# Kernel optimization log

Measured on AMD Instinct MI355X. Metric: run time of the kernel, lower is better.

The kernel has to match this reference:

```python
import jax, jax.numpy as jnp
import numpy as np

B, S, D = 2, 2048, 1024
H, HD = 16, 64


def setup_inputs() -> dict:
    key = jax.random.key(0)
    ks = jax.random.split(key, 10)
    scale = 1.0 / np.sqrt(D)
    inputs_q = jax.random.normal(ks[0], (B, S, D), dtype=jnp.float32)
    inputs_kv = jax.random.normal(ks[1], (B, S, D), dtype=jnp.float32)
    # causal mask, broadcast over batch: True = attend
    mask = jnp.broadcast_to(jnp.tril(jnp.ones((S, S), dtype=bool)), (B, S, S))
    Wq = jax.random.normal(ks[2], (D, H * HD), dtype=jnp.float32) * scale
    bq = jnp.zeros((H * HD,), dtype=jnp.float32)
    Wk = jax.random.normal(ks[3], (D, H * HD), dtype=jnp.float32) * scale
    bk = jnp.zeros((H * HD,), dtype=jnp.float32)
    Wv = jax.random.normal(ks[4], (D, H * HD), dtype=jnp.float32) * scale
    bv = jnp.zeros((H * HD,), dtype=jnp.float32)
    Wo = jax.random.normal(ks[5], (H * HD, D), dtype=jnp.float32) * scale
    bo = jnp.zeros((D,), dtype=jnp.float32)
    return {"inputs_q": inputs_q, "inputs_kv": inputs_kv, "mask": mask,
            "Wq": Wq, "bq": bq, "Wk": Wk, "bk": bk, "Wv": Wv, "bv": bv,
            "Wo": Wo, "bo": bo}


def reference(inputs_q, inputs_kv, mask, Wq, bq, Wk, bk, Wv, bv, Wo, bo):
    b, s_q, _ = inputs_q.shape
    s_k = inputs_kv.shape[1]
    # projections -> [B, S, H, HD]
    q = (inputs_q @ Wq + bq).reshape(b, s_q, H, HD)
    k = (inputs_kv @ Wk + bk).reshape(b, s_k, H, HD)
    v = (inputs_kv @ Wv + bv).reshape(b, s_k, H, HD)
    q = q / jnp.sqrt(jnp.asarray(HD, dtype=q.dtype))
    # scores: [B, H, Sq, Sk]
    attn = jnp.einsum('bqhd,bkhd->bhqk', q, k)
    m = mask[:, None, :, :]  # [B,1,Sq,Sk] broadcast over heads
    attn = jnp.where(m, attn, jnp.asarray(-1e30, dtype=attn.dtype))
    attn = jax.nn.softmax(attn, axis=-1)
    # dropout_rate = 0.0, deterministic -> identity
    out = jnp.einsum('bhqk,bkhd->bqhd', attn, v).reshape(b, s_q, H * HD)
    return out @ Wo + bo
```

## Files before the change

kernel.cpp:

```cpp
#include <hip/hip_runtime.h>

typedef __attribute__((ext_vector_type(4))) float f32x4;
typedef __attribute__((ext_vector_type(8))) short bf16x8;
typedef unsigned short u16;
typedef unsigned int u32;

#define AS1 __attribute__((address_space(1)))
#define AS3 __attribute__((address_space(3)))

#define WAITVM(N) do{ asm volatile("s_waitcnt vmcnt(" #N ")" ::: "memory"); \
                      __builtin_amdgcn_sched_barrier(0); }while(0)
#define RAWBAR    do{ __builtin_amdgcn_s_barrier();                          \
                      __builtin_amdgcn_sched_barrier(0); }while(0)

__device__ __forceinline__ float fast_exp2(float x){
  return __builtin_amdgcn_exp2f(x);
}

__device__ __forceinline__ u16 f2bf(float x){
  u32 u = __float_as_uint(x);
  u += 0x7fffu + ((u >> 16) & 1u);
  return (u16)(u >> 16);
}
__device__ __forceinline__ u16 f2bf_fast(float x){
  return (u16)((__float_as_uint(x) + 0x8000u) >> 16);
}

__global__ __launch_bounds__(256) void cvt_qkv(const float* __restrict__ s0,
                                               const float* __restrict__ s1,
                                               u16* __restrict__ d0,
                                               u16* __restrict__ d1, int n4)
{
  int i = blockIdx.x * 256 + threadIdx.x;
  if (i >= n4) return;
  const float* src = blockIdx.y ? s1 : s0;
  u16* dst = blockIdx.y ? d1 : d0;
  float4 v = reinterpret_cast<const float4*>(src)[i];
  ushort4 o;
  o.x = f2bf(v.x); o.y = f2bf(v.y); o.z = f2bf(v.z); o.w = f2bf(v.w);
  reinterpret_cast<ushort4*>(dst)[i] = o;
}

__global__ __launch_bounds__(256) void transpose_cvt4(const float* __restrict__ W0,
                                                      const float* __restrict__ W1,
                                                      const float* __restrict__ W2,
                                                      const float* __restrict__ W3,
                                                      u16* __restrict__ dst)
{
  __shared__ float tile[32][33];
  const int z = blockIdx.z;
  const float* src = z == 0 ? W0 : z == 1 ? W1 : z == 2 ? W2 : W3;
  u16* d = dst + (size_t)z * 1024 * 1024;
  int tx = threadIdx.x & 31, ty = threadIdx.x >> 5;
  int k0 = blockIdx.x * 32, n0 = blockIdx.y * 32;
  for (int r = 0; r < 4; ++r)
    tile[ty + r * 8][tx] = src[(size_t)(k0 + ty + r * 8) * 1024 + n0 + tx];
  __syncthreads();
  for (int r = 0; r < 4; ++r)
    d[(size_t)(n0 + ty + r * 8) * 1024 + k0 + tx] = f2bf(tile[tx][ty + r * 8]);
}

__global__ __launch_bounds__(256) void gemm_qkv(const u16* __restrict__ Xq,
                                                const u16* __restrict__ Xkv,
                                                const u16* __restrict__ Wt,
                                                const float* __restrict__ bq,
                                                const float* __restrict__ bk,
                                                const float* __restrict__ bv,
                                                u16* __restrict__ Qb,
                                                u16* __restrict__ Kb,
                                                u16* __restrict__ Vt,
                                                int M, int K)
{
  __shared__ u16 lA[3][128 * 32];
  __shared__ u16 lB[3][128 * 32];
  const int tid = threadIdx.x;
  const int l = tid & 63, w = tid >> 6;
  const int wr = w >> 1, wc = w & 1;
  const int bm0 = blockIdx.x * 128, bn0 = blockIdx.y * 128;
  const int seg = bn0 >> 10;
  const int nloc0 = bn0 & 1023;
  const u16* A = seg ? Xkv : Xq;
  const float* bias = seg == 0 ? bq : seg == 1 ? bk : bv;
  const float scale = seg == 0 ? 0.125f * 1.44269504089f : 1.0f;
  const int lr = l & 15, lg = (l >> 4) * 8;

#define STAGE_G(BI, KK) do{                                                   \
  _Pragma("unroll") for (int c_ = 0; c_ < 2; ++c_){                           \
    int e_ = (c_ * 256 + tid) * 8;                                            \
    int row_ = e_ >> 5, col_ = e_ & 31;                                       \
    __builtin_amdgcn_global_load_lds(                                         \
        (const AS1 u32*)(A + (size_t)(bm0 + row_) * K + (KK) * 32 + col_),    \
        (AS3 u32*)(&lA[BI][e_]), 16, 0, 0);                                   \
    __builtin_amdgcn_global_load_lds(                                         \
        (const AS1 u32*)(Wt + (size_t)(bn0 + row_) * K + (KK) * 32 + col_),   \
        (AS3 u32*)(&lB[BI][e_]), 16, 0, 0);                                   \
  }                                                                           \
}while(0)

  f32x4 acc[4][4];
#pragma unroll
  for (int m = 0; m < 4; ++m)
#pragma unroll
    for (int n = 0; n < 4; ++n) acc[m][n] = (f32x4){0.f, 0.f, 0.f, 0.f};

  STAGE_G(0, 0);
  STAGE_G(1, 1);

#pragma unroll
  for (int k = 0; k < 32; ++k){
    const int cur = k % 3;
    if (k < 30){ STAGE_G((k + 2) % 3, k + 2); WAITVM(8); }
    else if (k == 30){ WAITVM(4); }
    else { WAITVM(0); }
    RAWBAR;

    bf16x8 aF[4], bF[4];
#pragma unroll
    for (int m = 0; m < 4; ++m)
      aF[m] = *reinterpret_cast<const bf16x8*>(&lA[cur][(wr * 64 + m * 16 + lr) * 32 + lg]);
#pragma unroll
    for (int n = 0; n < 4; ++n)
      bF[n] = *reinterpret_cast<const bf16x8*>(&lB[cur][(wc * 64 + n * 16 + lr) * 32 + lg]);
    __builtin_amdgcn_s_setprio(1);
#pragma unroll
    for (int m = 0; m < 4; ++m)
#pragma unroll
      for (int n = 0; n < 4; ++n)
        acc[m][n] = __builtin_amdgcn_mfma_f32_16x16x32_bf16(aF[m], bF[n], acc[m][n], 0, 0, 0);
    __builtin_amdgcn_s_setprio(0);
    RAWBAR;
  }
#undef STAGE_G

  const int r0 = (l >> 4) * 4;
  if (seg < 2){
    u16* C = seg == 0 ? Qb : Kb;
#pragma unroll
    for (int m = 0; m < 4; ++m)
#pragma unroll
      for (int n = 0; n < 4; ++n){
        int col = nloc0 + wc * 64 + n * 16 + lr;
        float bv_ = bias[col];
#pragma unroll
        for (int r = 0; r < 4; ++r){
          int row = bm0 + wr * 64 + m * 16 + r0 + r;
          C[(size_t)row * 1024 + col] = f2bf((acc[m][n][r] + bv_) * scale);
        }
      }
  } else {
#pragma unroll
    for (int m = 0; m < 4; ++m)
#pragma unroll
      for (int n = 0; n < 4; ++n){
        int col = nloc0 + wc * 64 + n * 16 + lr;
        float bv_ = bias[col];
        int h = col >> 6, hdl = col & 63;
#pragma unroll
        for (int r = 0; r < 4; ++r){
          int row = bm0 + wr * 64 + m * 16 + r0 + r;
          int b = row >> 11, kv = row & 2047;
          size_t off = ((size_t)(b * 16 + h)) * 131072 + (size_t)hdl * 2048 + kv;
          Vt[off] = f2bf(acc[m][n][r] + bv_);
        }
      }
  }
}

__global__ __launch_bounds__(256) void gemm_out(const u16* __restrict__ A,
                                                const u16* __restrict__ Bt,
                                                const float* __restrict__ bias,
                                                float* __restrict__ Cf,
                                                int M, int N, int K)
{
  __shared__ u16 lA[3][64 * 32];
  __shared__ u16 lB[3][128 * 32];
  const int tid = threadIdx.x;
  const int l = tid & 63, w = tid >> 6;
  const int wr = w >> 1, wc = w & 1;
  const int bm0 = blockIdx.x * 64, bn0 = blockIdx.y * 128;
  const int lr = l & 15, lg = (l >> 4) * 8;

#define STAGE_O(BI, KK) do{                                                   \
  {                                                                           \
    int e_ = tid * 8;                                                         \
    int row_ = e_ >> 5, col_ = e_ & 31;                                       \
    __builtin_amdgcn_global_load_lds(                                         \
        (const AS1 u32*)(A + (size_t)(bm0 + row_) * K + (KK) * 32 + col_),    \
        (AS3 u32*)(&lA[BI][e_]), 16, 0, 0);                                   \
  }                                                                           \
  _Pragma("unroll") for (int c_ = 0; c_ < 2; ++c_){                           \
    int e_ = (c_ * 256 + tid) * 8;                                            \
    int row_ = e_ >> 5, col_ = e_ & 31;                                       \
    __builtin_amdgcn_global_load_lds(                                         \
        (const AS1 u32*)(Bt + (size_t)(bn0 + row_) * K + (KK) * 32 + col_),   \
        (AS3 u32*)(&lB[BI][e_]), 16, 0, 0);                                   \
  }                                                                           \
}while(0)

  f32x4 acc[2][4];
#pragma unroll
  for (int m = 0; m < 2; ++m)
#pragma unroll
    for (int n = 0; n < 4; ++n) acc[m][n] = (f32x4){0.f, 0.f, 0.f, 0.f};

  STAGE_O(0, 0);
  STAGE_O(1, 1);

#pragma unroll
  for (int k = 0; k < 32; ++k){
    const int cur = k % 3;
    if (k < 30){ STAGE_O((k + 2) % 3, k + 2); WAITVM(6); }
    else if (k == 30){ WAITVM(3); }
    else { WAITVM(0); }
    RAWBAR;

    bf16x8 aF[2], bF[4];
#pragma unroll
    for (int m = 0; m < 2; ++m)
      aF[m] = *reinterpret_cast<const bf16x8*>(&lA[cur][(wr * 32 + m * 16 + lr) * 32 + lg]);
#pragma unroll
    for (int n = 0; n < 4; ++n)
      bF[n] = *reinterpret_cast<const bf16x8*>(&lB[cur][(wc * 64 + n * 16 + lr) * 32 + lg]);
    __builtin_amdgcn_s_setprio(1);
#pragma unroll
    for (int m = 0; m < 2; ++m)
#pragma unroll
      for (int n = 0; n < 4; ++n)
        acc[m][n] = __builtin_amdgcn_mfma_f32_16x16x32_bf16(aF[m], bF[n], acc[m][n], 0, 0, 0);
    __builtin_amdgcn_s_setprio(0);
    RAWBAR;
  }
#undef STAGE_O

  const int r0 = (l >> 4) * 4;
#pragma unroll
  for (int m = 0; m < 2; ++m)
#pragma unroll
    for (int n = 0; n < 4; ++n){
      int col = bn0 + wc * 64 + n * 16 + lr;
      float bv_ = bias[col];
#pragma unroll
      for (int r = 0; r < 4; ++r){
        int row = bm0 + wr * 32 + m * 16 + r0 + r;
        Cf[(size_t)row * N + col] = acc[m][n][r] + bv_;
      }
    }
}

__global__ __launch_bounds__(512, 2) void attn_fwd(const u16* __restrict__ Qb,
                                                   const u16* __restrict__ Kb,
                                                   const u16* __restrict__ Vt,
                                                   u16* __restrict__ AO, int S)
{
  __shared__ u16 lK[2][64 * 64];
  __shared__ u16 lV[2][64 * 64];
  __shared__ u16 lP[8][16 * 72];
  const int tid = threadIdx.x, l = tid & 63, w = tid >> 6;
  const int j = blockIdx.x;
  const int xcd = j & 7;
  const int bh = xcd * 4 + ((j >> 3) & 3);
  const int p = j >> 5;
  const int bb = bh >> 4;
  const size_t baseQK = ((size_t)bb * S) * 1024 + (bh & 15) * 64;
  const u16* gK = Kb + baseQK;
  const u16* gV = Vt + (size_t)bh * 131072;
  const int lr = l & 15, g4 = l >> 4, lg = g4 * 8;

  u16* lPw = (u16*)lP[w];
  bf16x8 ones;
#pragma unroll
  for (int i = 0; i < 8; ++i) ones[i] = (short)0x3F80;

#define STAGE_KV(T, BI) do{                                                   \
  int row_ = tid >> 3, ch_ = tid & 7, sc_ = (ch_ ^ (row_ & 7)) * 8;           \
  __builtin_amdgcn_global_load_lds(                                           \
      (const AS1 u32*)(gK + (size_t)(64 * (T) + row_) * 1024 + sc_),          \
      (AS3 u32*)(&lK[BI][tid * 8]), 16, 0, 0);                                \
  __builtin_amdgcn_global_load_lds(                                           \
      (const AS1 u32*)(gV + (size_t)row_ * 2048 + 64 * (T) + sc_),            \
      (AS3 u32*)(&lV[BI][tid * 8]), 16, 0, 0);                                \
}while(0)

#pragma unroll
  for (int pass = 0; pass < 2; ++pass){
    const int qt = pass ? (15 - p) : p;
    const int ntb = 2 * qt + 2;
    const int q0 = qt * 128 + w * 16;

    bf16x8 qf[2];
#pragma unroll
    for (int kc = 0; kc < 2; ++kc)
      qf[kc] = *reinterpret_cast<const bf16x8*>(
          Qb + baseQK + (size_t)(q0 + lr) * 1024 + kc * 32 + lg);

    f32x4 acc_o[4], acc_l;
    acc_l = (f32x4){0.f, 0.f, 0.f, 0.f};
#pragma unroll
    for (int n = 0; n < 4; ++n) acc_o[n] = (f32x4){0.f, 0.f, 0.f, 0.f};

    int buf = 0;
    STAGE_KV(0, 0);
    for (int t = 0; t < ntb; ++t){
      if (t + 1 < ntb){ STAGE_KV(t + 1, buf ^ 1); WAITVM(2); }
      else            { WAITVM(0); }
      RAWBAR;

      if (64 * t <= q0 + 15){
        const u16* lKb = lK[buf];
        const u16* lVb = lV[buf];
        f32x4 sA[4];
#pragma unroll
        for (int np = 0; np < 4; ++np) sA[np] = (f32x4){0.f, 0.f, 0.f, 0.f};
        __builtin_amdgcn_s_setprio(1);
#pragma unroll
        for (int kc = 0; kc < 2; ++kc)
#pragma unroll
          for (int np = 0; np < 4; ++np){
            int row = np * 16 + lr, ch = kc * 4 + g4;
            bf16x8 kf = *reinterpret_cast<const bf16x8*>(
                reinterpret_cast<const char*>(lKb) + row * 128 + ((ch ^ (row & 7)) << 4));
            sA[np] = __builtin_amdgcn_mfma_f32_16x16x32_bf16(qf[kc], kf, sA[np], 0, 0, 0);
          }
        __builtin_amdgcn_s_setprio(0);

        const bool needmask = (64 * t + 63 > q0);
        if (needmask){
#pragma unroll
          for (int np = 0; np < 4; ++np){
            int kvg = 64 * t + np * 16 + lr;
#pragma unroll
            for (int r = 0; r < 4; ++r){
              int qg = q0 + g4 * 4 + r;
              float e = fast_exp2(sA[np][r]);
              lPw[(g4 * 4 + r) * 72 + np * 16 + lr] = f2bf_fast((kvg <= qg) ? e : 0.f);
            }
          }
        } else {
#pragma unroll
          for (int np = 0; np < 4; ++np)
#pragma unroll
            for (int r = 0; r < 4; ++r)
              lPw[(g4 * 4 + r) * 72 + np * 16 + lr] = f2bf_fast(fast_exp2(sA[np][r]));
        }

        bf16x8 pf[2];
#pragma unroll
        for (int kc = 0; kc < 2; ++kc)
          pf[kc] = *reinterpret_cast<const bf16x8*>(
              reinterpret_cast<const char*>(lPw) + lr * 144 + (kc * 4 + g4) * 16);
        __builtin_amdgcn_s_setprio(1);
#pragma unroll
        for (int kc = 0; kc < 2; ++kc){
          acc_l = __builtin_amdgcn_mfma_f32_16x16x32_bf16(pf[kc], ones, acc_l, 0, 0, 0);
#pragma unroll
          for (int n = 0; n < 4; ++n){
            int row = n * 16 + lr, ch = kc * 4 + g4;
            bf16x8 vf = *reinterpret_cast<const bf16x8*>(
                reinterpret_cast<const char*>(lVb) + row * 128 + ((ch ^ (row & 7)) << 4));
            acc_o[n] = __builtin_amdgcn_mfma_f32_16x16x32_bf16(pf[kc], vf, acc_o[n], 0, 0, 0);
          }
        }
        __builtin_amdgcn_s_setprio(0);
      }
      RAWBAR;
      buf ^= 1;
    }

    float inv[4];
#pragma unroll
    for (int r = 0; r < 4; ++r) inv[r] = 1.0f / acc_l[r];
#pragma unroll
    for (int n = 0; n < 4; ++n)
#pragma unroll
      for (int r = 0; r < 4; ++r){
        int row = q0 + g4 * 4 + r;
        AO[baseQK + (size_t)row * 1024 + n * 16 + lr] = f2bf(acc_o[n][r] * inv[r]);
      }
  }
#undef STAGE_KV
}

extern "C" void kernel_launch(void* const* d_in, const int* in_sizes, int n_in,
                              void* d_out, int out_size, void* d_ws, size_t ws_size,
                              hipStream_t stream)
{
  const float* inq  = (const float*)d_in[0];
  const float* inkv = (const float*)d_in[1];
  const float* Wq = (const float*)d_in[3];
  const float* bq = (const float*)d_in[4];
  const float* Wk = (const float*)d_in[5];
  const float* bk = (const float*)d_in[6];
  const float* Wv = (const float*)d_in[7];
  const float* bv = (const float*)d_in[8];
  const float* Wo = (const float*)d_in[9];
  const float* bo = (const float*)d_in[10];
  float* out = (float*)d_out;

  const int B = 2, S = 2048, D = 1024;
  const int M = B * S;

  char* ws = (char*)d_ws;
  const size_t MB = 1024ull * 1024ull;
  u16* Xq  = (u16*)(ws + 0 * MB);
  u16* Xkv = (u16*)(ws + 8 * MB);
  u16* Wt  = (u16*)(ws + 16 * MB);
  u16* Wot = (u16*)(ws + 22 * MB);
  u16* Qb  = (u16*)(ws + 24 * MB);
  u16* Kb  = (u16*)(ws + 32 * MB);
  u16* Vtg = (u16*)(ws + 40 * MB);
  u16* AOb = (u16*)(ws + 48 * MB);

  cvt_qkv<<<dim3(M * D / 4 / 256, 2), 256, 0, stream>>>(inq, inkv, Xq, Xkv, M * D / 4);

  transpose_cvt4<<<dim3(32, 32, 4), 256, 0, stream>>>(Wq, Wk, Wv, Wo, Wt);

  gemm_qkv<<<dim3(M / 128, 3072 / 128), 256, 0, stream>>>(Xq, Xkv, Wt, bq, bk, bv,
                                                          Qb, Kb, Vtg, M, D);

  attn_fwd<<<dim3(256), 512, 0, stream>>>(Qb, Kb, Vtg, AOb, S);

  gemm_out<<<dim3(M / 64, D / 128), 256, 0, stream>>>(AOb, Wot, bo, out, M, D, D);
}
```

Measured before the change: 119.0 us.

## Merge conversion kernels into one prep launch and enlarge QKV GEMM tiles

The input-activation bf16 conversion and the weight transpose-convert are combined into a single kernel, with blocks dispatched by blockIdx.z, which removes one launch. The QKV projection GEMM moves from 128x128 tiles with 4 waves to 256x256 tiles with 8 waves, each wave computing a 128x64 sub-tile. This raises operand reuse per LDS load and halves global traffic per output, at the cost of more LDS (96KB triple buffered), more accumulator registers, and only 192 blocks, which may leave part of the GPU idle.

```diff
diff --git a/kernel.cpp b/kernel.cpp
--- a/kernel.cpp
+++ b/kernel.cpp
@@ -26,57 +26,60 @@
   return (u16)((__float_as_uint(x) + 0x8000u) >> 16);
 }
 
-__global__ __launch_bounds__(256) void cvt_qkv(const float* __restrict__ s0,
-                                               const float* __restrict__ s1,
-                                               u16* __restrict__ d0,
-                                               u16* __restrict__ d1, int n4)
+__global__ __launch_bounds__(256) void prep(const float* __restrict__ W0,
+                                            const float* __restrict__ W1,
+                                            const float* __restrict__ W2,
+                                            const float* __restrict__ W3,
+                                            u16* __restrict__ Wt,
+                                            const float* __restrict__ inq,
+                                            const float* __restrict__ inkv,
+                                            u16* __restrict__ Xq,
+                                            u16* __restrict__ Xkv)
 {
-  int i = blockIdx.x * 256 + threadIdx.x;
-  if (i >= n4) return;
-  const float* src = blockIdx.y ? s1 : s0;
-  u16* dst = blockIdx.y ? d1 : d0;
-  float4 v = reinterpret_cast<const float4*>(src)[i];
-  ushort4 o;
-  o.x = f2bf(v.x); o.y = f2bf(v.y); o.z = f2bf(v.z); o.w = f2bf(v.w);
-  reinterpret_cast<ushort4*>(dst)[i] = o;
-}
-
-__global__ __launch_bounds__(256) void transpose_cvt4(const float* __restrict__ W0,
-                                                      const float* __restrict__ W1,
-                                                      const float* __restrict__ W2,
-                                                      const float* __restrict__ W3,
-                                                      u16* __restrict__ dst)
+  const int z = blockIdx.z;
+  if (z < 4){
+    __shared__ float tile[32][33];
+    const float* src = z == 0 ? W0 : z == 1 ? W1 : z == 2 ? W2 : W3;
+    u16* d = Wt + (size_t)z * 1024 * 1024;
+    int tx = threadIdx.x & 31, ty = threadIdx.x >> 5;
+    int k0 = blockIdx.x * 32, n0 = blockIdx.y * 32;
+    for (int r = 0; r < 4; ++r)
+      tile[ty + r * 8][tx] = src[(size_t)(k0 + ty + r * 8) * 1024 + n0 + tx];
+    __syncthreads();
+    for (int r = 0; r < 4; ++r)
+      d[(size_t)(n0 + ty + r * 8) * 1024 + k0 + tx] = f2bf(tile[tx][ty + r * 8]);
+  } else {
+    const float* src = z == 4 ? inq : inkv;
+    u16* dst = z == 4 ? Xq : Xkv;
+    int bid = blockIdx.y * 32 + blockIdx.x;
+    size_t base4 = ((size_t)bid * 256 + threadIdx.x) * 4;
+#pragma unroll
+    for (int i = 0; i < 4; ++i){
+      float4 v = reinterpret_cast<const float4*>(src)[base4 + i];
+      ushort4 o;
+      o.x = f2bf(v.x); o.y = f2bf(v.y); o.z = f2bf(v.z); o.w = f2bf(v.w);
+      reinterpret_cast<ushort4*>(dst)[base4 + i] = o;
+    }
+  }
+}
+
+__global__ __launch_bounds__(512, 2) void gemm_qkv(const u16* __restrict__ Xq,
+                                                   const u16* __restrict__ Xkv,
+                                                   const u16* __restrict__ Wt,
+                                                   const float* __restrict__ bq,
+                                                   const float* __restrict__ bk,
+                                                   const float* __restrict__ bv,
+                                                   u16* __restrict__ Qb,
+                                                   u16* __restrict__ Kb,
+                                                   u16* __restrict__ Vt,
+                                                   int M, int K)
 {
-  __shared__ float tile[32][33];
-  const int z = blockIdx.z;
-  const float* src = z == 0 ? W0 : z == 1 ? W1 : z == 2 ? W2 : W3;
-  u16* d = dst + (size_t)z * 1024 * 1024;
-  int tx = threadIdx.x & 31, ty = threadIdx.x >> 5;
-  int k0 = blockIdx.x * 32, n0 = blockIdx.y * 32;
-  for (int r = 0; r < 4; ++r)
-    tile[ty + r * 8][tx] = src[(size_t)(k0 + ty + r * 8) * 1024 + n0 + tx];
-  __syncthreads();
-  for (int r = 0; r < 4; ++r)
-    d[(size_t)(n0 + ty + r * 8) * 1024 + k0 + tx] = f2bf(tile[tx][ty + r * 8]);
-}
-
-__global__ __launch_bounds__(256) void gemm_qkv(const u16* __restrict__ Xq,
-                                                const u16* __restrict__ Xkv,
-                                                const u16* __restrict__ Wt,
-                                                const float* __restrict__ bq,
-                                                const float* __restrict__ bk,
-                                                const float* __restrict__ bv,
-                                                u16* __restrict__ Qb,
-                                                u16* __restrict__ Kb,
-                                                u16* __restrict__ Vt,
-                                                int M, int K)
-{
-  __shared__ u16 lA[3][128 * 32];
-  __shared__ u16 lB[3][128 * 32];
+  __shared__ u16 lA[3][256 * 32];
+  __shared__ u16 lB[3][256 * 32];
   const int tid = threadIdx.x;
   const int l = tid & 63, w = tid >> 6;
-  const int wr = w >> 1, wc = w & 1;
-  const int bm0 = blockIdx.x * 128, bn0 = blockIdx.y * 128;
+  const int wr = w >> 2, wc = w & 3;
+  const int bm0 = blockIdx.x * 256, bn0 = blockIdx.y * 256;
   const int seg = bn0 >> 10;
   const int nloc0 = bn0 & 1023;
   const u16* A = seg ? Xkv : Xq;
@@ -86,7 +89,7 @@
 
 #define STAGE_G(BI, KK) do{                                                   \
   _Pragma("unroll") for (int c_ = 0; c_ < 2; ++c_){                           \
-    int e_ = (c_ * 256 + tid) * 8;                                            \
+    int e_ = (c_ * 512 + tid) * 8;                                            \
     int row_ = e_ >> 5, col_ = e_ & 31;                                       \
     __builtin_amdgcn_global_load_lds(                                         \
         (const AS1 u32*)(A + (size_t)(bm0 + row_) * K + (KK) * 32 + col_),    \
@@ -97,9 +100,9 @@
   }                                                                           \
 }while(0)
 
-  f32x4 acc[4][4];
-#pragma unroll
-  for (int m = 0; m < 4; ++m)
+  f32x4 acc[8][4];
+#pragma unroll
+  for (int m = 0; m < 8; ++m)
 #pragma unroll
     for (int n = 0; n < 4; ++n) acc[m][n] = (f32x4){0.f, 0.f, 0.f, 0.f};
 
@@ -114,16 +117,16 @@
     else { WAITVM(0); }
     RAWBAR;
 
-    bf16x8 aF[4], bF[4];
-#pragma unroll
-    for (int m = 0; m < 4; ++m)
-      aF[m] = *reinterpret_cast<const bf16x8*>(&lA[cur][(wr * 64 + m * 16 + lr) * 32 + lg]);
+    bf16x8 aF[8], bF[4];
+#pragma unroll
+    for (int m = 0; m < 8; ++m)
+      aF[m] = *reinterpret_cast<const bf16x8*>(&lA[cur][(wr * 128 + m * 16 + lr) * 32 + lg]);
 #pragma unroll
     for (int n = 0; n < 4; ++n)
       bF[n] = *reinterpret_cast<const bf16x8*>(&lB[cur][(wc * 64 + n * 16 + lr) * 32 + lg]);
     __builtin_amdgcn_s_setprio(1);
 #pragma unroll
-    for (int m = 0; m < 4; ++m)
+    for (int m = 0; m < 8; ++m)
 #pragma unroll
       for (int n = 0; n < 4; ++n)
         acc[m][n] = __builtin_amdgcn_mfma_f32_16x16x32_bf16(aF[m], bF[n], acc[m][n], 0, 0, 0);
@@ -136,20 +139,20 @@
   if (seg < 2){
     u16* C = seg == 0 ? Qb : Kb;
 #pragma unroll
-    for (int m = 0; m < 4; ++m)
+    for (int m = 0; m < 8; ++m)
 #pragma unroll
       for (int n = 0; n < 4; ++n){
         int col = nloc0 + wc * 64 + n * 16 + lr;
         float bv_ = bias[col];
 #pragma unroll
         for (int r = 0; r < 4; ++r){
-          int row = bm0 + wr * 64 + m * 16 + r0 + r;
+          int row = bm0 + wr * 128 + m * 16 + r0 + r;
           C[(size_t)row * 1024 + col] = f2bf((acc[m][n][r] + bv_) * scale);
         }
       }
   } else {
 #pragma unroll
-    for (int m = 0; m < 4; ++m)
+    for (int m = 0; m < 8; ++m)
 #pragma unroll
       for (int n = 0; n < 4; ++n){
         int col = nloc0 + wc * 64 + n * 16 + lr;
@@ -157,7 +160,7 @@
         int h = col >> 6, hdl = col & 63;
 #pragma unroll
         for (int r = 0; r < 4; ++r){
-          int row = bm0 + wr * 64 + m * 16 + r0 + r;
+          int row = bm0 + wr * 128 + m * 16 + r0 + r;
           int b = row >> 11, kv = row & 2047;
           size_t off = ((size_t)(b * 16 + h)) * 131072 + (size_t)hdl * 2048 + kv;
           Vt[off] = f2bf(acc[m][n][r] + bv_);
@@ -410,11 +413,9 @@
   u16* Vtg = (u16*)(ws + 40 * MB);
   u16* AOb = (u16*)(ws + 48 * MB);
 
-  cvt_qkv<<<dim3(M * D / 4 / 256, 2), 256, 0, stream>>>(inq, inkv, Xq, Xkv, M * D / 4);
-
-  transpose_cvt4<<<dim3(32, 32, 4), 256, 0, stream>>>(Wq, Wk, Wv, Wo, Wt);
-
-  gemm_qkv<<<dim3(M / 128, 3072 / 128), 256, 0, stream>>>(Xq, Xkv, Wt, bq, bk, bv,
+  prep<<<dim3(32, 32, 6), 256, 0, stream>>>(Wq, Wk, Wv, Wo, Wt, inq, inkv, Xq, Xkv);
+
+  gemm_qkv<<<dim3(M / 256, 3072 / 256), 512, 0, stream>>>(Xq, Xkv, Wt, bq, bk, bv,
                                                           Qb, Kb, Vtg, M, D);
 
   attn_fwd<<<dim3(256), 512, 0, stream>>>(Qb, Kb, Vtg, AOb, S);
```

New measurement: 117.2 us. No clear change (-1.5%).
